# Kernel tuning notes

Measured on AMD Instinct MI355X. Metric: run time of the kernel, lower is better.

The kernel has to match this reference:

```python
import jax, jax.numpy as jnp
import numpy as np

TEMPERATURE = 0.07
KNN_AUG = True
NUM_NEIGHBORS = 10
B, N, D = 2048, 65536, 128
NUM_CLUSTERS = 100
EPS = 1e-12


def _l2_normalize(x):
    # matches torch F.normalize(dim=1): x / max(||x||, eps)
    norm = jnp.sqrt(jnp.sum(x * x, axis=1, keepdims=True))
    return x / jnp.maximum(norm, EPS)


def setup_inputs() -> dict:
    key = jax.random.key(0)
    k1, k2, k3, k4 = jax.random.split(key, 4)
    return {
        "features": jax.random.normal(k1, (B, D), dtype=jnp.float32),
        "cluster_idxes": jax.random.randint(k2, (B,), 0, NUM_CLUSTERS),
        "global_features": jax.random.normal(k3, (N, D), dtype=jnp.float32),
        "global_clusters": jax.random.randint(k4, (N,), 0, NUM_CLUSTERS),
    }


def reference(features, cluster_idxes, global_features, global_clusters):
    f = _l2_normalize(features)            # [B, D]
    g = _l2_normalize(global_features)     # [N, D]
    sim = (f @ g.T) / TEMPERATURE          # [B, N]

    # cluster-membership positive mask: [B, N]
    pos_mask = (cluster_idxes[:, None] == global_clusters[None, :]).astype(sim.dtype)

    if KNN_AUG:
        k_val = min(NUM_NEIGHBORS, sim.shape[-1])
        _, knn_idx = jax.lax.top_k(sim, k_val)  # [B, k]
        rows = jnp.arange(sim.shape[0])[:, None]
        knn_mask = jnp.zeros_like(pos_mask).at[rows, knn_idx].set(1.0)
        pos_mask = ((pos_mask + knn_mask) > 0).astype(sim.dtype)

    # masked log-softmax reduction (same math as original: exp/sum/log)
    log_prob = sim - jnp.log(jnp.sum(jnp.exp(sim), axis=1, keepdims=True) + EPS)  # [B, N]
    mean_log_prob_pos = jnp.sum(pos_mask * log_prob, axis=1) / (jnp.sum(pos_mask, axis=1) + EPS)
    return -jnp.mean(mean_log_prob_pos)
```

## Files before the change

### kernel.cpp

```cpp
#include <hip/hip_runtime.h>

#define B_ROWS 2048
#define N_GLB  65536
#define DDIM   128
#define NCLUST 100
#define INV_T  (1.0f/0.07f)
#define LOG2E  1.4426950408889634f
#define LN2    0.6931471805599453f
#define NSPLIT 16
#define CHUNK_COLS (N_GLB/NSPLIT)
#define ITERS (CHUNK_COLS/64)
#define ROWSB 16
#define GRPB 2048
#define TOPK 10
#define CAP  256
#define NSLICE 8
#define TAU_L2E (3.7881f*LOG2E)
#define CSC    65536.0f
#define INV_CSC (1.0f/65536.0f)

typedef __attribute__((ext_vector_type(4))) float f32x4;
typedef __attribute__((ext_vector_type(2))) long lg2;
typedef unsigned long long u64;

__device__ __forceinline__ unsigned fmono(float v) {
  unsigned u = __float_as_uint(v);
  return ((int)u < 0) ? ~u : (u | 0x80000000u);
}
__device__ __forceinline__ float fmono_inv(unsigned m) {
  unsigned u = (m & 0x80000000u) ? (m & 0x7FFFFFFFu) : ~m;
  return __uint_as_float(u);
}
__device__ __forceinline__ u64 mkkey(float val, int col) {
  return ((u64)fmono(val) << 32) | (unsigned)(~(unsigned)col);
}
__device__ __forceinline__ u64 umax64(u64 a, u64 b) { return a > b ? a : b; }

__device__ __forceinline__ float fp8d(unsigned b) {
  unsigned e = (b >> 3) & 15, m = b & 7;
  float v = e ? __uint_as_float(((e + 120u) << 23) | (m << 20))
              : (float)m * 0.001953125f;
  return (b & 0x80u) ? -v : v;
}

__global__ __launch_bounds__(256) void prep_kernel(
    const float* __restrict__ f, const float* __restrict__ g,
    char* __restrict__ wsf2, char* __restrict__ wsg2,
    float* __restrict__ inv_fT, float* __restrict__ inv_g) {
  __shared__ unsigned short lds[1024];
  const int t = threadIdx.x, lane = t & 63, w = t >> 6;
  const int grp = blockIdx.x;
  const bool isf = grp < (B_ROWS / 16);

  #pragma unroll
  for (int j = 0; j < 4; ++j) {
    int rit = w * 4 + j;
    int row = grp * 16 + rit;
    int rr = isf ? row : row - B_ROWS;
    const float* src = (isf ? f : g) + (size_t)rr * DDIM;
    float2 v = ((const float2*)src)[lane];
    float ss = v.x * v.x + v.y * v.y;
    #pragma unroll
    for (int m = 32; m; m >>= 1) ss += __shfl_xor(ss, m);
    float inv = 1.0f / fmaxf(sqrtf(ss), 1e-12f);
    if (lane == 0) { if (isf) inv_fT[rr] = inv * INV_T; else inv_g[rr] = inv; }
    float sc = isf ? inv * (INV_T * LOG2E) : inv;
    unsigned pk = __builtin_amdgcn_cvt_pk_fp8_f32(v.x * sc, v.y * sc, 0u, false);
    int k = 2 * lane;
    int off = ((k >> 6) << 10) + (((k >> 3) & 3) << 8) + (rit << 4)
            + (((k >> 5) & 1) << 3) + (k & 7);
    lds[off >> 1] = (unsigned short)(pk & 0xFFFFu);
  }
  __syncthreads();
  char* dst = isf ? (wsf2 + (size_t)grp * GRPB)
                  : (wsg2 + (size_t)(grp - B_ROWS / 16) * GRPB);
  if (t < 128) ((uint4*)dst)[t] = ((const uint4*)lds)[t];
}

__global__ __launch_bounds__(256) void csum2_kernel(
    const float* __restrict__ g, const int* __restrict__ gclust,
    const float* __restrict__ inv_g,
    int* __restrict__ csum_i32, int* __restrict__ hist8) {
  __shared__ int cs[NCLUST * DDIM];
  __shared__ int hcnt[NCLUST];
  const int t = threadIdx.x, lane = t & 63, w = t >> 6;
  for (int i = t; i < NCLUST * DDIM; i += 256) cs[i] = 0;
  if (t < NCLUST) hcnt[t] = 0;
  __syncthreads();

  const int rbase = blockIdx.x * 512;
  const int rg = lane >> 4;
  const int ch = lane & 15;
  for (int step = 0; step < 32; ++step) {
    int row = rbase + step * 16 + w * 4 + rg;
    int c = gclust[row];
    float scale = inv_g[row] * CSC;
    const float* gp = g + (size_t)row * DDIM + 8 * ch;
    float4 a = *(const float4*)gp;
    float4 b = *(const float4*)(gp + 4);
    int* dst = &cs[c * DDIM + ch * 8];
    atomicAdd(dst + 0, (int)rintf(a.x * scale));
    atomicAdd(dst + 1, (int)rintf(a.y * scale));
    atomicAdd(dst + 2, (int)rintf(a.z * scale));
    atomicAdd(dst + 3, (int)rintf(a.w * scale));
    atomicAdd(dst + 4, (int)rintf(b.x * scale));
    atomicAdd(dst + 5, (int)rintf(b.y * scale));
    atomicAdd(dst + 6, (int)rintf(b.z * scale));
    atomicAdd(dst + 7, (int)rintf(b.w * scale));
    if (ch == 0) atomicAdd(&hcnt[c], 1);
  }
  __syncthreads();
  const int slice = blockIdx.x & (NSLICE - 1);
  for (int i = t; i < NCLUST * DDIM; i += 256) {
    int x = cs[i];
    if (x) atomicAdd(&csum_i32[(size_t)slice * NCLUST * DDIM + i], x);
  }
  if (t < NCLUST && hcnt[t]) atomicAdd(&hist8[slice * 128 + t], hcnt[t]);
}

#define PUSHQ(av, q)                                                            \
  if ((av) > TAU_L2E) {                                                         \
    int rw = r0 + lhi * 4 + (q);                                                \
    int slot = atomicAdd(&cnt[rw], 1);                                          \
    if (slot < CAP) { lv[rw * CAP + slot] = (av) * LN2; li[rw * CAP + slot] = colv; } \
  }

#define LOADB(dst, gptr)                                                        \
  { dst[0] = *(const uint4*)((gptr) + (size_t)lane * 16);                       \
    dst[1] = *(const uint4*)((gptr) + 1024 + (size_t)lane * 16); }

#define COMPUTE_REFILL(bb, itv, refbase, dorefill)                              \
  {                                                                             \
    f32x4 acA = {0,0,0,0}, acB = {0,0,0,0};                                     \
    lg2 bs0 = __builtin_bit_cast(lg2, bb[0]);                                   \
    lg2 bs1 = __builtin_bit_cast(lg2, bb[1]);                                   \
    if (dorefill) {                                                             \
      bb[0] = *(const uint4*)((refbase) + (size_t)lane * 16);                   \
      bb[1] = *(const uint4*)((refbase) + 1024 + (size_t)lane * 16);            \
    }                                                                           \
    acA = __builtin_amdgcn_mfma_f32_16x16x32_fp8_fp8(afr[0][0], bs0[0], acA, 0, 0, 0); \
    acB = __builtin_amdgcn_mfma_f32_16x16x32_fp8_fp8(afr[1][0], bs1[0], acB, 0, 0, 0); \
    acA = __builtin_amdgcn_mfma_f32_16x16x32_fp8_fp8(afr[0][1], bs0[1], acA, 0, 0, 0); \
    acB = __builtin_amdgcn_mfma_f32_16x16x32_fp8_fp8(afr[1][1], bs1[1], acB, 0, 0, 0); \
    f32x4 a = acA + acB;                                                        \
    se.x += __builtin_amdgcn_exp2f(a.x);                                        \
    se.y += __builtin_amdgcn_exp2f(a.y);                                        \
    se.z += __builtin_amdgcn_exp2f(a.z);                                        \
    se.w += __builtin_amdgcn_exp2f(a.w);                                        \
    float mx = fmaxf(fmaxf(a.x, a.y), fmaxf(a.z, a.w));                         \
    if (mx > TAU_L2E) {                                                         \
      const int colv = chunk * CHUNK_COLS + (itv) * 64 + w * 16 + l15;          \
      PUSHQ(a.x, 0) PUSHQ(a.y, 1) PUSHQ(a.z, 2) PUSHQ(a.w, 3)                   \
    }                                                                           \
  }

__global__ __launch_bounds__(256, 8) void sim_kernel(
    const char* __restrict__ wsf2, const char* __restrict__ wsg2,
    float* __restrict__ p_se, float* __restrict__ lv, int* __restrict__ li,
    int* __restrict__ cnt) {
  __shared__ float sered[4][ROWSB];
  const int t = threadIdx.x, lane = t & 63, w = t >> 6;
  const int l15 = lane & 15, lhi = lane >> 4;
  const int chunk = blockIdx.x;
  const int r0 = blockIdx.y * ROWSB;

  const char* fbase = wsf2 + (size_t)(r0 >> 4) * GRPB;
  lg2 afr[2];
  #pragma unroll
  for (int sp = 0; sp < 2; ++sp)
    afr[sp] = __builtin_bit_cast(lg2,
      *(const uint4*)(fbase + sp * 1024 + (size_t)lane * 16));

  f32x4 se = {0.f, 0.f, 0.f, 0.f};

  const char* gb = wsg2 + (size_t)(chunk * (CHUNK_COLS / 16) + w) * GRPB;
  uint4 b0[2], b1[2];
  LOADB(b0, gb)
  LOADB(b1, gb + 8192)
  for (int it = 0; it < ITERS; it += 2) {
    COMPUTE_REFILL(b0, it,     gb + 2 * 8192, it + 2 < ITERS)
    COMPUTE_REFILL(b1, it + 1, gb + 3 * 8192, it + 3 < ITERS)
    gb += 2 * 8192;
  }

  #pragma unroll
  for (int q = 0; q < 4; ++q) {
    float s = se[q];
    s += __shfl_xor(s, 1); s += __shfl_xor(s, 2);
    s += __shfl_xor(s, 4); s += __shfl_xor(s, 8);
    if (l15 == 0) sered[w][lhi * 4 + q] = s;
  }
  __syncthreads();
  if (t < ROWSB) {
    float s = sered[0][t] + sered[1][t] + sered[2][t] + sered[3][t];
    p_se[(size_t)(r0 + t) * NSPLIT + chunk] = s;
  }
}

__global__ __launch_bounds__(256) void merge_kernel(
    const float* __restrict__ f, const int* __restrict__ fclust,
    const int* __restrict__ gclust, const float* __restrict__ inv_fT,
    const float* __restrict__ p_se, const int* __restrict__ csum_i32,
    const int* __restrict__ hist8, const float* __restrict__ lv,
    const int* __restrict__ li, const int* __restrict__ cnt,
    const char* __restrict__ wsf2, const char* __restrict__ wsg2,
    float* __restrict__ rowv) {
  const int lane = threadIdx.x & 63, w = threadIdx.x >> 6;
  const int r = blockIdx.x * 4 + w;

  float sev = (lane < NSPLIT) ? p_se[(size_t)r * NSPLIT + lane] : 0.f;
  sev += __shfl_xor(sev, 8); sev += __shfl_xor(sev, 4);
  sev += __shfl_xor(sev, 2); sev += __shfl_xor(sev, 1);
  sev = __shfl(sev, 0);

  int rc = fclust[r];
  float2 fv = ((const float2*)(f + (size_t)r * DDIM))[lane];
  float sc = inv_fT[r];
  int ia = 0, ib = 0, hc = 0;
  #pragma unroll
  for (int s = 0; s < NSLICE; ++s) {
    ia += csum_i32[(size_t)s * NCLUST * DDIM + rc * DDIM + 2 * lane];
    ib += csum_i32[(size_t)s * NCLUST * DDIM + rc * DDIM + 2 * lane + 1];
    hc += hist8[s * 128 + rc];
  }
  float dt = fv.x * sc * (ia * INV_CSC) + fv.y * sc * (ib * INV_CSC);
  #pragma unroll
  for (int m = 32; m; m >>= 1) dt += __shfl_xor(dt, m);
  dt = __shfl(dt, 0);

  float Cc = (float)hc;
  int n = cnt[r];
  bool bad = (n < TOPK) || (n > CAP);
  float S10 = 0.f, C10 = 0.f;
  if (!bad) {
    u64 k0 = 0, k1 = 0, k2 = 0, k3 = 0;
    int e = lane;
    if (e < n) k0 = mkkey(lv[(size_t)r * CAP + e], li[(size_t)r * CAP + e]);
    e = lane + 64;
    if (e < n) k1 = mkkey(lv[(size_t)r * CAP + e], li[(size_t)r * CAP + e]);
    e = lane + 128;
    if (e < n) k2 = mkkey(lv[(size_t)r * CAP + e], li[(size_t)r * CAP + e]);
    e = lane + 192;
    if (e < n) k3 = mkkey(lv[(size_t)r * CAP + e], li[(size_t)r * CAP + e]);
    for (int it = 0; it < TOPK; ++it) {
      u64 best = umax64(umax64(k0, k1), umax64(k2, k3));
      #pragma unroll
      for (int m = 32; m; m >>= 1) best = umax64(best, __shfl_xor(best, m));
      float val = fmono_inv((unsigned)(best >> 32));
      int col = (int)(~(unsigned)(best & 0xFFFFFFFFull));
      int gc = gclust[col];
      if (gc != rc) { S10 += val; C10 += 1.f; }
      if (k0 == best) k0 = 0;
      if (k1 == best) k1 = 0;
      if (k2 == best) k2 = 0;
      if (k3 == best) k3 = 0;
    }
  } else {
    uint4 fr[8];
    #pragma unroll
    for (int pc = 0; pc < 8; ++pc)
      fr[pc] = *(const uint4*)(wsf2 + (size_t)(r >> 4) * GRPB + (pc >> 2) * 1024
                               + (pc & 3) * 256 + (r & 15) * 16);
    u64 tk[TOPK];
    #pragma unroll
    for (int i = 0; i < TOPK; ++i) tk[i] = 0;
    for (int col = lane; col < N_GLB; col += 64) {
      const char* gp = wsg2 + (size_t)(col >> 4) * GRPB + (col & 15) * 16;
      float acc = 0.f;
      #pragma unroll
      for (int pc = 0; pc < 8; ++pc) {
        uint4 gv = *(const uint4*)(gp + (pc >> 2) * 1024 + (pc & 3) * 256);
        uint4 fc = fr[pc];
        #pragma unroll
        for (int wd = 0; wd < 4; ++wd) {
          unsigned fa = (&fc.x)[wd], ga = (&gv.x)[wd];
          #pragma unroll
          for (int b = 0; b < 4; ++b)
            acc += fp8d((fa >> (8 * b)) & 0xFFu) * fp8d((ga >> (8 * b)) & 0xFFu);
        }
      }
      u64 key = mkkey(acc, col);
      if (key > tk[0]) {
        u64 cur = key;
        #pragma unroll
        for (int i = 0; i < TOPK - 1; ++i) {
          u64 nxt = tk[i + 1];
          u64 lo = cur < nxt ? cur : nxt;
          u64 hi = cur < nxt ? nxt : cur;
          tk[i] = lo; cur = hi;
        }
        tk[TOPK - 1] = cur;
      }
    }
    for (int it = 0; it < TOPK; ++it) {
      u64 best = tk[TOPK - 1];
      #pragma unroll
      for (int m = 32; m; m >>= 1) best = umax64(best, __shfl_xor(best, m));
      float val = fmono_inv((unsigned)(best >> 32)) * LN2;
      int col = (int)(~(unsigned)(best & 0xFFFFFFFFull));
      if (gclust[col] != rc) { S10 += val; C10 += 1.f; }
      if (tk[TOPK - 1] == best) {
        #pragma unroll
        for (int i = TOPK - 1; i > 0; --i) tk[i] = tk[i - 1];
        tk[0] = 0;
      }
    }
  }
  if (lane == 0) {
    float L = logf(sev + 1e-12f);
    float C = Cc + C10;
    rowv[r] = (dt + S10 - C * L) / (C + 1e-12f);
  }
}

__global__ void final_kernel(const float* __restrict__ rowv, float* __restrict__ out) {
  __shared__ float sm[256];
  int t = threadIdx.x;
  float s = 0.f;
  for (int i = t; i < B_ROWS; i += 256) s += rowv[i];
  sm[t] = s;
  __syncthreads();
  for (int o = 128; o; o >>= 1) { if (t < o) sm[t] += sm[t + o]; __syncthreads(); }
  if (t == 0) out[0] = -(sm[0] / (float)B_ROWS);
}

extern "C" void kernel_launch(void* const* d_in, const int* in_sizes, int n_in,
                              void* d_out, int out_size, void* d_ws, size_t ws_size,
                              hipStream_t stream) {
  const float* f  = (const float*)d_in[0];
  const int*   fc = (const int*)  d_in[1];
  const float* g  = (const float*)d_in[2];
  const int*   gc = (const int*)  d_in[3];
  float* out = (float*)d_out;

  char* ws = (char*)d_ws;
  char*  wsf2    = ws;
  char*  wsg2    = ws + 262144;
  float* inv_fT  = (float*)(ws + 8650752);
  float* inv_g   = (float*)(ws + 8658944);
  float* p_se    = (float*)(ws + 8921088);
  int*   csum_i32= (int*)  (ws + 9052160);
  int*   hist8   = (int*)  (ws + 9461760);
  int*   cnt     = (int*)  (ws + 9465856);
  float* lv      = (float*)(ws + 9474048);
  int*   li      = (int*)  (ws + 11571200);
  float* rowv    = (float*)(ws + 13668352);

  hipMemsetAsync(ws + 9052160, 0, 421888, stream);

  prep_kernel<<<(B_ROWS + N_GLB) / 16, 256, 0, stream>>>(f, g, wsf2, wsg2,
                                                         inv_fT, inv_g);

  csum2_kernel<<<N_GLB / 512, 256, 0, stream>>>(g, gc, inv_g, csum_i32, hist8);

  dim3 grid(NSPLIT, B_ROWS / ROWSB);
  sim_kernel<<<grid, 256, 0, stream>>>(wsf2, wsg2, p_se, lv, li, cnt);

  merge_kernel<<<B_ROWS / 4, 256, 0, stream>>>(f, fc, gc, inv_fT, p_se, csum_i32,
                                               hist8, lv, li, cnt, wsf2, wsg2, rowv);
  final_kernel<<<1, 256, 0, stream>>>(rowv, out);
}
```

Before: 116.3 us.

## Reuse B fragments across two row tiles, fold memset and final reduce

```diff
diff --git a/kernel.cpp b/kernel.cpp
--- a/kernel.cpp
+++ b/kernel.cpp
@@ -9,8 +9,8 @@
 #define LN2    0.6931471805599453f
 #define NSPLIT 16
 #define CHUNK_COLS (N_GLB/NSPLIT)
-#define ITERS (CHUNK_COLS/64)
-#define ROWSB 16
+#define ITERS (CHUNK_COLS/(16*8))
+#define ROWSB 32
 #define GRPB 2048
 #define TOPK 10
 #define CAP  256
@@ -18,6 +18,7 @@
 #define TAU_L2E (3.7881f*LOG2E)
 #define CSC    65536.0f
 #define INV_CSC (1.0f/65536.0f)
+#define ZWORDS 105476
 
 typedef __attribute__((ext_vector_type(4))) float f32x4;
 typedef __attribute__((ext_vector_type(2))) long lg2;
@@ -46,11 +47,21 @@
 __global__ __launch_bounds__(256) void prep_kernel(
     const float* __restrict__ f, const float* __restrict__ g,
     char* __restrict__ wsf2, char* __restrict__ wsg2,
-    float* __restrict__ inv_fT, float* __restrict__ inv_g) {
+    float* __restrict__ inv_fT, float* __restrict__ inv_g,
+    unsigned* __restrict__ zbase) {
   __shared__ unsigned short lds[1024];
   const int t = threadIdx.x, lane = t & 63, w = t >> 6;
   const int grp = blockIdx.x;
   const bool isf = grp < (B_ROWS / 16);
+
+  if (isf) {
+    int gid = grp * 256 + t;
+    #pragma unroll
+    for (int k = 0; k < 4; ++k) {
+      int idx = gid + k * 32768;
+      if (idx < ZWORDS) zbase[idx] = 0u;
+    }
+  }
 
   #pragma unroll
   for (int j = 0; j < 4; ++j) {
@@ -118,11 +129,21 @@
   if (t < NCLUST && hcnt[t]) atomicAdd(&hist8[slice * 128 + t], hcnt[t]);
 }
 
-#define PUSHQ(av, q)                                                            \
+#define PUSHQ(av, mm, q)                                                        \
   if ((av) > TAU_L2E) {                                                         \
-    int rw = r0 + lhi * 4 + (q);                                                \
+    int rw = r0 + (mm) * 16 + lhi * 4 + (q);                                    \
     int slot = atomicAdd(&cnt[rw], 1);                                          \
     if (slot < CAP) { lv[rw * CAP + slot] = (av) * LN2; li[rw * CAP + slot] = colv; } \
+  }
+
+#define EPI(a, mm)                                                              \
+  {                                                                             \
+    se[mm].x += __builtin_amdgcn_exp2f(a.x);                                    \
+    se[mm].y += __builtin_amdgcn_exp2f(a.y);                                    \
+    se[mm].z += __builtin_amdgcn_exp2f(a.z);                                    \
+    se[mm].w += __builtin_amdgcn_exp2f(a.w);                                    \
+    float mx = fmaxf(fmaxf(a.x, a.y), fmaxf(a.z, a.w));                         \
+    if (mx > TAU_L2E) { PUSHQ(a.x, mm, 0) PUSHQ(a.y, mm, 1) PUSHQ(a.z, mm, 2) PUSHQ(a.w, mm, 3) } \
   }
 
 #define LOADB(dst, gptr)                                                        \
@@ -131,68 +152,71 @@
 
 #define COMPUTE_REFILL(bb, itv, refbase, dorefill)                              \
   {                                                                             \
-    f32x4 acA = {0,0,0,0}, acB = {0,0,0,0};                                     \
+    f32x4 ac0 = {0,0,0,0}, ac1 = {0,0,0,0};                                     \
     lg2 bs0 = __builtin_bit_cast(lg2, bb[0]);                                   \
     lg2 bs1 = __builtin_bit_cast(lg2, bb[1]);                                   \
     if (dorefill) {                                                             \
       bb[0] = *(const uint4*)((refbase) + (size_t)lane * 16);                   \
       bb[1] = *(const uint4*)((refbase) + 1024 + (size_t)lane * 16);            \
     }                                                                           \
-    acA = __builtin_amdgcn_mfma_f32_16x16x32_fp8_fp8(afr[0][0], bs0[0], acA, 0, 0, 0); \
-    acB = __builtin_amdgcn_mfma_f32_16x16x32_fp8_fp8(afr[1][0], bs1[0], acB, 0, 0, 0); \
-    acA = __builtin_amdgcn_mfma_f32_16x16x32_fp8_fp8(afr[0][1], bs0[1], acA, 0, 0, 0); \
-    acB = __builtin_amdgcn_mfma_f32_16x16x32_fp8_fp8(afr[1][1], bs1[1], acB, 0, 0, 0); \
-    f32x4 a = acA + acB;                                                        \
-    se.x += __builtin_amdgcn_exp2f(a.x);                                        \
-    se.y += __builtin_amdgcn_exp2f(a.y);                                        \
-    se.z += __builtin_amdgcn_exp2f(a.z);                                        \
-    se.w += __builtin_amdgcn_exp2f(a.w);                                        \
-    float mx = fmaxf(fmaxf(a.x, a.y), fmaxf(a.z, a.w));                         \
-    if (mx > TAU_L2E) {                                                         \
-      const int colv = chunk * CHUNK_COLS + (itv) * 64 + w * 16 + l15;          \
-      PUSHQ(a.x, 0) PUSHQ(a.y, 1) PUSHQ(a.z, 2) PUSHQ(a.w, 3)                   \
-    }                                                                           \
-  }
-
-__global__ __launch_bounds__(256, 8) void sim_kernel(
+    ac0 = __builtin_amdgcn_mfma_f32_16x16x32_fp8_fp8(afr[0][0][0], bs0[0], ac0, 0, 0, 0); \
+    ac1 = __builtin_amdgcn_mfma_f32_16x16x32_fp8_fp8(afr[1][0][0], bs0[0], ac1, 0, 0, 0); \
+    ac0 = __builtin_amdgcn_mfma_f32_16x16x32_fp8_fp8(afr[0][0][1], bs0[1], ac0, 0, 0, 0); \
+    ac1 = __builtin_amdgcn_mfma_f32_16x16x32_fp8_fp8(afr[1][0][1], bs0[1], ac1, 0, 0, 0); \
+    ac0 = __builtin_amdgcn_mfma_f32_16x16x32_fp8_fp8(afr[0][1][0], bs1[0], ac0, 0, 0, 0); \
+    ac1 = __builtin_amdgcn_mfma_f32_16x16x32_fp8_fp8(afr[1][1][0], bs1[0], ac1, 0, 0, 0); \
+    ac0 = __builtin_amdgcn_mfma_f32_16x16x32_fp8_fp8(afr[0][1][1], bs1[1], ac0, 0, 0, 0); \
+    ac1 = __builtin_amdgcn_mfma_f32_16x16x32_fp8_fp8(afr[1][1][1], bs1[1], ac1, 0, 0, 0); \
+    const int colv = chunk * CHUNK_COLS + ((itv) * 8 + w) * 16 + l15;           \
+    EPI(ac0, 0) EPI(ac1, 1)                                                     \
+  }
+
+__global__ __launch_bounds__(512, 8) void sim_kernel(
     const char* __restrict__ wsf2, const char* __restrict__ wsg2,
     float* __restrict__ p_se, float* __restrict__ lv, int* __restrict__ li,
     int* __restrict__ cnt) {
-  __shared__ float sered[4][ROWSB];
+  __shared__ float sered[8][ROWSB];
   const int t = threadIdx.x, lane = t & 63, w = t >> 6;
   const int l15 = lane & 15, lhi = lane >> 4;
   const int chunk = blockIdx.x;
   const int r0 = blockIdx.y * ROWSB;
 
   const char* fbase = wsf2 + (size_t)(r0 >> 4) * GRPB;
-  lg2 afr[2];
-  #pragma unroll
-  for (int sp = 0; sp < 2; ++sp)
-    afr[sp] = __builtin_bit_cast(lg2,
-      *(const uint4*)(fbase + sp * 1024 + (size_t)lane * 16));
-
-  f32x4 se = {0.f, 0.f, 0.f, 0.f};
+  lg2 afr[2][2];
+  #pragma unroll
+  for (int m = 0; m < 2; ++m)
+    #pragma unroll
+    for (int sp = 0; sp < 2; ++sp)
+      afr[m][sp] = __builtin_bit_cast(lg2,
+        *(const uint4*)(fbase + (size_t)m * GRPB + sp * 1024 + (size_t)lane * 16));
+
+  f32x4 z = {0.f, 0.f, 0.f, 0.f};
+  f32x4 se[2] = {z, z};
 
   const char* gb = wsg2 + (size_t)(chunk * (CHUNK_COLS / 16) + w) * GRPB;
   uint4 b0[2], b1[2];
   LOADB(b0, gb)
-  LOADB(b1, gb + 8192)
+  LOADB(b1, gb + 8 * GRPB)
   for (int it = 0; it < ITERS; it += 2) {
-    COMPUTE_REFILL(b0, it,     gb + 2 * 8192, it + 2 < ITERS)
-    COMPUTE_REFILL(b1, it + 1, gb + 3 * 8192, it + 3 < ITERS)
-    gb += 2 * 8192;
-  }
-
-  #pragma unroll
-  for (int q = 0; q < 4; ++q) {
-    float s = se[q];
-    s += __shfl_xor(s, 1); s += __shfl_xor(s, 2);
-    s += __shfl_xor(s, 4); s += __shfl_xor(s, 8);
-    if (l15 == 0) sered[w][lhi * 4 + q] = s;
-  }
+    COMPUTE_REFILL(b0, it,     gb + 16 * GRPB, it + 2 < ITERS)
+    COMPUTE_REFILL(b1, it + 1, gb + 24 * GRPB, it + 3 < ITERS)
+    gb += 16 * GRPB;
+  }
+
+  #pragma unroll
+  for (int m = 0; m < 2; ++m)
+    #pragma unroll
+    for (int q = 0; q < 4; ++q) {
+      float s = se[m][q];
+      s += __shfl_xor(s, 1); s += __shfl_xor(s, 2);
+      s += __shfl_xor(s, 4); s += __shfl_xor(s, 8);
+      if (l15 == 0) sered[w][m * 16 + lhi * 4 + q] = s;
+    }
   __syncthreads();
   if (t < ROWSB) {
-    float s = sered[0][t] + sered[1][t] + sered[2][t] + sered[3][t];
+    float s = 0.f;
+    #pragma unroll
+    for (int i = 0; i < 8; ++i) s += sered[i][t];
     p_se[(size_t)(r0 + t) * NSPLIT + chunk] = s;
   }
 }
@@ -204,7 +228,8 @@
     const int* __restrict__ hist8, const float* __restrict__ lv,
     const int* __restrict__ li, const int* __restrict__ cnt,
     const char* __restrict__ wsf2, const char* __restrict__ wsg2,
-    float* __restrict__ rowv) {
+    u64* __restrict__ sum64, unsigned* __restrict__ done,
+    float* __restrict__ out) {
   const int lane = threadIdx.x & 63, w = threadIdx.x >> 6;
   const int r = blockIdx.x * 4 + w;
 
@@ -309,19 +334,19 @@
   if (lane == 0) {
     float L = logf(sev + 1e-12f);
     float C = Cc + C10;
-    rowv[r] = (dt + S10 - C * L) / (C + 1e-12f);
-  }
-}
-
-__global__ void final_kernel(const float* __restrict__ rowv, float* __restrict__ out) {
-  __shared__ float sm[256];
-  int t = threadIdx.x;
-  float s = 0.f;
-  for (int i = t; i < B_ROWS; i += 256) s += rowv[i];
-  sm[t] = s;
-  __syncthreads();
-  for (int o = 128; o; o >>= 1) { if (t < o) sm[t] += sm[t + o]; __syncthreads(); }
-  if (t == 0) out[0] = -(sm[0] / (float)B_ROWS);
+    float mlpp = (dt + S10 - C * L) / (C + 1e-12f);
+    long long q = (long long)llrintf(mlpp * 1048576.0f);
+    atomicAdd(sum64, (u64)q);
+  }
+  __syncthreads();
+  if (threadIdx.x == 0) {
+    __threadfence();
+    unsigned old = atomicAdd(done, 1u);
+    if (old == gridDim.x - 1) {
+      u64 s = atomicAdd(sum64, 0ULL);
+      out[0] = (float)(-((double)(long long)s / 1048576.0 / (double)B_ROWS));
+    }
+  }
 }
 
 extern "C" void kernel_launch(void* const* d_in, const int* in_sizes, int n_in,
@@ -342,21 +367,21 @@
   int*   csum_i32= (int*)  (ws + 9052160);
   int*   hist8   = (int*)  (ws + 9461760);
   int*   cnt     = (int*)  (ws + 9465856);
-  float* lv      = (float*)(ws + 9474048);
-  int*   li      = (int*)  (ws + 11571200);
-  float* rowv    = (float*)(ws + 13668352);
-
-  hipMemsetAsync(ws + 9052160, 0, 421888, stream);
+  u64*   sum64   = (u64*)  (ws + 9474048);
+  unsigned* done = (unsigned*)(ws + 9474056);
+  unsigned* zbase= (unsigned*)(ws + 9052160);
+  float* lv      = (float*)(ws + 9474304);
+  int*   li      = (int*)  (ws + 11571456);
 
   prep_kernel<<<(B_ROWS + N_GLB) / 16, 256, 0, stream>>>(f, g, wsf2, wsg2,
-                                                         inv_fT, inv_g);
+                                                         inv_fT, inv_g, zbase);
 
   csum2_kernel<<<N_GLB / 512, 256, 0, stream>>>(g, gc, inv_g, csum_i32, hist8);
 
   dim3 grid(NSPLIT, B_ROWS / ROWSB);
-  sim_kernel<<<grid, 256, 0, stream>>>(wsf2, wsg2, p_se, lv, li, cnt);
+  sim_kernel<<<grid, 512, 0, stream>>>(wsf2, wsg2, p_se, lv, li, cnt);
 
   merge_kernel<<<B_ROWS / 4, 256, 0, stream>>>(f, fc, gc, inv_fT, p_se, csum_i32,
-                                               hist8, lv, li, cnt, wsf2, wsg2, rowv);
-  final_kernel<<<1, 256, 0, stream>>>(rowv, out);
-}
+                                               hist8, lv, li, cnt, wsf2, wsg2,
+                                               sum64, done, out);
+}
```

Measured after the change: 180.2 us. 54.9% more time.
